# Optimization experiments

Measured on AMD Instinct MI355X. Metric: run time of the kernel, lower is better.

Reference implementation:

```python
import jax, jax.numpy as jnp
import numpy as np

def setup_inputs() -> dict:
    key = jax.random.key(0)
    k1, k2, k3, k4 = jax.random.split(key, 4)
    B, T, D = 4, 4096, 256
    # xavier_normal_ with gain 0.002: std = 0.002 * sqrt(2/(D+D))
    std = 0.002 * np.sqrt(2.0 / (D + D))
    return {
        "x": jax.random.normal(k1, (B, T, D), dtype=jnp.float32),
        "W_k": jax.random.normal(k2, (D, D), dtype=jnp.float32) * std,
        "W_q": jax.random.normal(k3, (D, D), dtype=jnp.float32) * std,
        "W_v": jax.random.normal(k4, (D, D), dtype=jnp.float32) * std,
    }

def reference(x, W_k, W_q, W_v):
    # Projections: (B,T,D) @ (D,D) -> (B,T,D)
    K = jnp.einsum('btd,dk->btk', x, W_k)
    Q = jnp.einsum('btd,dq->btq', x, W_q)
    V = jnp.einsum('btd,dv->btv', x, W_v)
    # Note: original code has NO 1/sqrt(D) scaling.
    scores = jnp.einsum('bqd,bkd->bqk', Q, K)  # (B,T,T)
    attn = jax.nn.softmax(scores, axis=2)
    return jnp.einsum('bta,bav->btv', attn, V)
```

## Files before the change

### kernel.cpp

```cpp
#include <hip/hip_runtime.h>

typedef __attribute__((ext_vector_type(4))) float f32x4;
typedef __attribute__((ext_vector_type(8))) __bf16 bf16x8;
typedef __attribute__((ext_vector_type(4))) unsigned short u16x4;
typedef unsigned short u16;
typedef unsigned int u32;
typedef unsigned long long u64;

#define AS1 __attribute__((address_space(1)))
#define AS3 __attribute__((address_space(3)))

__device__ __forceinline__ void gload_lds16(const void* g, void* l) {
  __builtin_amdgcn_global_load_lds((const AS1 u32*)g, (AS3 u32*)l, 16, 0, 0);
}

__global__ __launch_bounds__(256) void k_flag(float* __restrict__ out, int n) {
  for (int i = blockIdx.x * 256 + threadIdx.x; i < n; i += gridDim.x * 256)
    out[i] = 1.0f;
}

__global__ __launch_bounds__(256) void k_cvt_w(const float* __restrict__ Wk,
                                               const float* __restrict__ Wq,
                                               const float* __restrict__ Wv,
                                               __bf16* __restrict__ Wt) {
  const float* W = blockIdx.y == 0 ? Wk : (blockIdx.y == 1 ? Wq : Wv);
  int i = blockIdx.x * 256 + threadIdx.x;
  int n = i >> 8, k = i & 255;
  Wt[blockIdx.y * 65536 + i] = (__bf16)W[k * 256 + n];
}

__global__ __launch_bounds__(256) void k_proj(const float* __restrict__ x,
                                              const __bf16* __restrict__ Wt,
                                              __bf16* __restrict__ Kb,
                                              __bf16* __restrict__ Qb,
                                              __bf16* __restrict__ Vt) {
  __shared__ __bf16 As[128][72];
  __shared__ __bf16 Bs[128][72];
  int tid = threadIdx.x;
  int lane = tid & 63, w = tid >> 6;
  int l15 = lane & 15, l4 = lane >> 4;
  int m0 = blockIdx.x * 128, n0 = blockIdx.y * 128;
  int z = blockIdx.z;
  const __bf16* Wz = Wt + z * 65536;
  int wm = (w & 1) * 64, wn = (w >> 1) * 64;
  f32x4 acc[4][4];
  for (int a = 0; a < 4; ++a)
    for (int b = 0; b < 4; ++b) acc[a][b] = (f32x4){0.f, 0.f, 0.f, 0.f};

  for (int k0 = 0; k0 < 256; k0 += 64) {
    __syncthreads();
    for (int it = 0; it < 4; ++it) {
      int id = it * 256 + tid, r = id >> 3, c = id & 7;
      const float* src = x + (u64)(m0 + r) * 256 + k0 + c * 8;
      f32x4 a = *(const f32x4*)src, b2 = *(const f32x4*)(src + 4);
      bf16x8 o;
      o[0] = (__bf16)a[0];  o[1] = (__bf16)a[1];  o[2] = (__bf16)a[2];  o[3] = (__bf16)a[3];
      o[4] = (__bf16)b2[0]; o[5] = (__bf16)b2[1]; o[6] = (__bf16)b2[2]; o[7] = (__bf16)b2[3];
      *(bf16x8*)&As[r][c * 8] = o;
    }
    for (int it = 0; it < 4; ++it) {
      int id = it * 256 + tid, r = id >> 3, c = id & 7;
      *(bf16x8*)&Bs[r][c * 8] = *(const bf16x8*)(Wz + (u64)(n0 + r) * 256 + k0 + c * 8);
    }
    __syncthreads();
    for (int ks = 0; ks < 2; ++ks) {
      bf16x8 af[4], bg[4];
      for (int mf = 0; mf < 4; ++mf)
        af[mf] = *(const bf16x8*)&As[wm + mf * 16 + l15][(ks * 4 + l4) * 8];
      for (int nf = 0; nf < 4; ++nf)
        bg[nf] = *(const bf16x8*)&Bs[wn + nf * 16 + l15][(ks * 4 + l4) * 8];
      for (int mf = 0; mf < 4; ++mf)
        for (int nf = 0; nf < 4; ++nf)
          acc[mf][nf] = __builtin_amdgcn_mfma_f32_16x16x32_bf16(af[mf], bg[nf],
                                                                acc[mf][nf], 0, 0, 0);
    }
  }
  if (z != 2) {
    __bf16* C = z == 0 ? Kb : Qb;
    for (int mf = 0; mf < 4; ++mf)
      for (int nf = 0; nf < 4; ++nf)
        for (int r = 0; r < 4; ++r) {
          int m = m0 + wm + mf * 16 + l4 * 4 + r;
          int n = n0 + wn + nf * 16 + l15;
          C[(u64)m * 256 + n] = (__bf16)acc[mf][nf][r];
        }
  } else {
    int bb = m0 >> 12;
    for (int mf = 0; mf < 4; ++mf)
      for (int nf = 0; nf < 4; ++nf) {
        int n = n0 + wn + nf * 16 + l15;
        int tb = (m0 & 4095) + wm + mf * 16 + l4 * 4;
        u16x4 pk;
        for (int r = 0; r < 4; ++r) {
          __bf16 h = (__bf16)acc[mf][nf][r];
          pk[r] = __builtin_bit_cast(u16, h);
        }
        *(u16x4*)(Vt + (u64)bb * 1048576 + (u64)n * 4096 + tb) = pk;
      }
  }
}

#define KVB 32
__global__ __launch_bounds__(256) void k_attn(const __bf16* __restrict__ Qb,
                                              const __bf16* __restrict__ Kb,
                                              const __bf16* __restrict__ Vt,
                                              float* __restrict__ Out) {
  extern __shared__ char smem[];
  __bf16* Ks0 = (__bf16*)smem;
  __bf16* Ks1 = (__bf16*)(smem + 16384);
  __bf16* Vs0 = (__bf16*)(smem + 32768);
  __bf16* Vs1 = (__bf16*)(smem + 49152);
  __bf16* Ps  = (__bf16*)(smem + 65536);
  float*  Ls  = (float*)(smem + 69632);
  int tid = threadIdx.x, lane = tid & 63, w = tid >> 6;
  int l15 = lane & 15, l4 = lane >> 4;
  int id8 = blockIdx.x & 7, slot = blockIdx.x >> 3;
  int b = id8 >> 1;
  int q0 = (((id8 & 1) << 5) | slot) << 6;
  const __bf16* Kbb = Kb + (u64)b * 4096 * 256;
  const __bf16* Vtb = Vt + (u64)b * 1048576;

  const __bf16* Qrow = Qb + (u64)(b * 4096 + q0 + w * 16 + l15) * 256;
  bf16x8 qf[8];
  for (int ks = 0; ks < 8; ++ks) qf[ks] = *(const bf16x8*)(Qrow + ks * 32 + l4 * 8);

  f32x4 oacc[4][4];
  for (int a = 0; a < 4; ++a)
    for (int c = 0; c < 4; ++c) oacc[a][c] = (f32x4){0.f, 0.f, 0.f, 0.f};
  float lp[4] = {0.f, 0.f, 0.f, 0.f};

  auto stageK = [&](int kv0, __bf16* dst) {
    for (int it = 0; it < 4; ++it) {
      int id = it * 256 + tid;
      int r = id >> 5, c = id & 31, sc = c ^ (r & 7);
      gload_lds16(Kbb + (u64)(kv0 + r) * 256 + sc * 8, (char*)dst + id * 16);
    }
  };
  auto stageV = [&](int kv0, __bf16* dst) {
    for (int it = 0; it < 4; ++it) {
      int id = it * 256 + tid;
      int d = id >> 2, c = id & 3, sc = c ^ (d & 3);
      gload_lds16(Vtb + (u64)d * 4096 + kv0 + sc * 8, (char*)dst + id * 16);
    }
  };

  stageK(0, Ks0);
  stageV(0, Vs0);
  asm volatile("s_waitcnt vmcnt(0)" ::: "memory");
  __syncthreads();

  for (int t = 0; t < 128; ++t) {
    __bf16* Kc = (t & 1) ? Ks1 : Ks0;
    __bf16* Vc = (t & 1) ? Vs1 : Vs0;
    __bf16* Kn = (t & 1) ? Ks0 : Ks1;
    __bf16* Vn = (t & 1) ? Vs0 : Vs1;
    if (t < 127) { stageK((t + 1) * KVB, Kn); stageV((t + 1) * KVB, Vn); }

    f32x4 s0a = (f32x4){0.f, 0.f, 0.f, 0.f}, s0b = s0a, s1a = s0a, s1b = s0a;
    for (int ks = 0; ks < 8; ks += 2) {
      int ch00 = (ks * 4 + l4) ^ (l15 & 7);
      int ch10 = (ks * 4 + l4) ^ ((16 + l15) & 7);
      int ch01 = ((ks + 1) * 4 + l4) ^ (l15 & 7);
      int ch11 = ((ks + 1) * 4 + l4) ^ ((16 + l15) & 7);
      bf16x8 kf00 = *(const bf16x8*)((const char*)Kc + l15 * 512 + ch00 * 16);
      bf16x8 kf10 = *(const bf16x8*)((const char*)Kc + (16 + l15) * 512 + ch10 * 16);
      bf16x8 kf01 = *(const bf16x8*)((const char*)Kc + l15 * 512 + ch01 * 16);
      bf16x8 kf11 = *(const bf16x8*)((const char*)Kc + (16 + l15) * 512 + ch11 * 16);
      s0a = __builtin_amdgcn_mfma_f32_16x16x32_bf16(qf[ks], kf00, s0a, 0, 0, 0);
      s1a = __builtin_amdgcn_mfma_f32_16x16x32_bf16(qf[ks], kf10, s1a, 0, 0, 0);
      s0b = __builtin_amdgcn_mfma_f32_16x16x32_bf16(qf[ks + 1], kf01, s0b, 0, 0, 0);
      s1b = __builtin_amdgcn_mfma_f32_16x16x32_bf16(qf[ks + 1], kf11, s1b, 0, 0, 0);
    }
    f32x4 s0 = s0a + s0b, s1 = s1a + s1b;

    for (int r = 0; r < 4; ++r) {
      float p0 = __expf(s0[r]);
      float p1 = __expf(s1[r]);
      lp[r] += p0 + p1;
      int row = w * 16 + l4 * 4 + r;
      int c0 = (l15 >> 3) ^ (row & 3);
      Ps[row * 32 + c0 * 8 + (l15 & 7)] = (__bf16)p0;
      int c1 = ((16 + l15) >> 3) ^ (row & 3);
      Ps[row * 32 + c1 * 8 + (l15 & 7)] = (__bf16)p1;
    }
    asm volatile("s_waitcnt lgkmcnt(0)\n\ts_barrier" ::: "memory");

    bf16x8 vf[4];
    for (int nf = 0; nf < 4; ++nf) {
      int d = w * 64 + nf * 16 + l15;
      int vc = l4 ^ (d & 3);
      vf[nf] = *(const bf16x8*)((const char*)Vc + d * 64 + vc * 16);
    }
    for (int mf = 0; mf < 4; ++mf) {
      int qr = mf * 16 + l15;
      int pc = l4 ^ (qr & 3);
      bf16x8 pa = *(const bf16x8*)(Ps + qr * 32 + pc * 8);
      for (int nf = 0; nf < 4; ++nf)
        oacc[mf][nf] = __builtin_amdgcn_mfma_f32_16x16x32_bf16(pa, vf[nf], oacc[mf][nf], 0, 0, 0);
    }
    asm volatile("s_waitcnt vmcnt(0) lgkmcnt(0)\n\ts_barrier" ::: "memory");
  }

  for (int m = 1; m < 16; m <<= 1)
    for (int r = 0; r < 4; ++r) lp[r] += __shfl_xor(lp[r], m, 64);
  if (l15 == 0)
    for (int r = 0; r < 4; ++r) Ls[w * 16 + l4 * 4 + r] = lp[r];
  __syncthreads();

  float* Ob = Out + (u64)(b * 4096 + q0) * 256;
  for (int mf = 0; mf < 4; ++mf)
    for (int r = 0; r < 4; ++r) {
      float inv = 1.0f / Ls[mf * 16 + l4 * 4 + r];
      for (int nf = 0; nf < 4; ++nf)
        Ob[(u64)(mf * 16 + l4 * 4 + r) * 256 + w * 64 + nf * 16 + l15] =
            oacc[mf][nf][r] * inv;
    }
}

extern "C" void kernel_launch(void* const* d_in, const int* in_sizes, int n_in,
                              void* d_out, int out_size, void* d_ws, size_t ws_size,
                              hipStream_t stream) {
  const float* x  = (const float*)d_in[0];
  const float* Wk = (const float*)d_in[1];
  const float* Wq = (const float*)d_in[2];
  const float* Wv = (const float*)d_in[3];
  float* out = (float*)d_out;
  char* ws = (char*)d_ws;

  const size_t NEEDED = 25559040;
  if (ws_size < NEEDED) {
    k_flag<<<1024, 256, 0, stream>>>(out, out_size);
    return;
  }
  __bf16* Wt = (__bf16*)ws;
  __bf16* Kb = (__bf16*)(ws + 393216);
  __bf16* Qb = (__bf16*)(ws + 8781824);
  __bf16* Vt = (__bf16*)(ws + 17170432);

  k_cvt_w<<<dim3(256, 3), 256, 0, stream>>>(Wk, Wq, Wv, Wt);
  k_proj<<<dim3(128, 2, 3), 256, 0, stream>>>(x, Wt, Kb, Qb, Vt);
  k_attn<<<256, 256, 69888, stream>>>(Qb, Kb, Vt, out);
}
```

Before: 232.6 us.

## Halve attention query tile to 32 rows and pre-convert x to bf16 with async LDS loads

The attention kernel now gives each block 32 query rows instead of 64, doubling the grid to 512 blocks. The four waves split into two query halves times two key halves, and the two partial row sums are combined at the end. The projection kernel now reads a bf16 copy of x, produced by a new conversion kernel into the output buffer used as scratch, and stages tiles into swizzled LDS with global_load_lds. The aim is better CU occupancy and cheaper projection loads. The cost is that every block reloads K and V for fewer queries, doubling K/V traffic, plus one extra kernel launch.

```diff
diff --git a/kernel.cpp b/kernel.cpp
--- a/kernel.cpp
+++ b/kernel.cpp
@@ -17,6 +17,17 @@
 __global__ __launch_bounds__(256) void k_flag(float* __restrict__ out, int n) {
   for (int i = blockIdx.x * 256 + threadIdx.x; i < n; i += gridDim.x * 256)
     out[i] = 1.0f;
+}
+
+__global__ __launch_bounds__(256) void k_cvt_x(const float* __restrict__ x,
+                                               __bf16* __restrict__ xb) {
+  int i = blockIdx.x * 256 + threadIdx.x;
+  const f32x4* p = (const f32x4*)x;
+  f32x4 a = p[i * 2], b = p[i * 2 + 1];
+  bf16x8 o;
+  o[0] = (__bf16)a[0]; o[1] = (__bf16)a[1]; o[2] = (__bf16)a[2]; o[3] = (__bf16)a[3];
+  o[4] = (__bf16)b[0]; o[5] = (__bf16)b[1]; o[6] = (__bf16)b[2]; o[7] = (__bf16)b[3];
+  ((bf16x8*)xb)[i] = o;
 }
 
 __global__ __launch_bounds__(256) void k_cvt_w(const float* __restrict__ Wk,
@@ -29,13 +40,13 @@
   Wt[blockIdx.y * 65536 + i] = (__bf16)W[k * 256 + n];
 }
 
-__global__ __launch_bounds__(256) void k_proj(const float* __restrict__ x,
+__global__ __launch_bounds__(256) void k_proj(const __bf16* __restrict__ xb,
                                               const __bf16* __restrict__ Wt,
                                               __bf16* __restrict__ Kb,
                                               __bf16* __restrict__ Qb,
                                               __bf16* __restrict__ Vt) {
-  __shared__ __bf16 As[128][72];
-  __shared__ __bf16 Bs[128][72];
+  __shared__ __bf16 As[128 * 64];
+  __shared__ __bf16 Bs[128 * 64];
   int tid = threadIdx.x;
   int lane = tid & 63, w = tid >> 6;
   int l15 = lane & 15, l4 = lane >> 4;
@@ -50,25 +61,29 @@
   for (int k0 = 0; k0 < 256; k0 += 64) {
     __syncthreads();
     for (int it = 0; it < 4; ++it) {
-      int id = it * 256 + tid, r = id >> 3, c = id & 7;
-      const float* src = x + (u64)(m0 + r) * 256 + k0 + c * 8;
-      f32x4 a = *(const f32x4*)src, b2 = *(const f32x4*)(src + 4);
-      bf16x8 o;
-      o[0] = (__bf16)a[0];  o[1] = (__bf16)a[1];  o[2] = (__bf16)a[2];  o[3] = (__bf16)a[3];
-      o[4] = (__bf16)b2[0]; o[5] = (__bf16)b2[1]; o[6] = (__bf16)b2[2]; o[7] = (__bf16)b2[3];
-      *(bf16x8*)&As[r][c * 8] = o;
-    }
-    for (int it = 0; it < 4; ++it) {
-      int id = it * 256 + tid, r = id >> 3, c = id & 7;
-      *(bf16x8*)&Bs[r][c * 8] = *(const bf16x8*)(Wz + (u64)(n0 + r) * 256 + k0 + c * 8);
-    }
+      int id = it * 256 + tid;
+      int r = id >> 3, c = id & 7, sc = c ^ (r & 7);
+      gload_lds16(xb + (u64)(m0 + r) * 256 + k0 + sc * 8, (char*)As + id * 16);
+    }
+    for (int it = 0; it < 4; ++it) {
+      int id = it * 256 + tid;
+      int r = id >> 3, c = id & 7, sc = c ^ (r & 7);
+      gload_lds16(Wz + (u64)(n0 + r) * 256 + k0 + sc * 8, (char*)Bs + id * 16);
+    }
+    asm volatile("s_waitcnt vmcnt(0)" ::: "memory");
     __syncthreads();
     for (int ks = 0; ks < 2; ++ks) {
       bf16x8 af[4], bg[4];
-      for (int mf = 0; mf < 4; ++mf)
-        af[mf] = *(const bf16x8*)&As[wm + mf * 16 + l15][(ks * 4 + l4) * 8];
-      for (int nf = 0; nf < 4; ++nf)
-        bg[nf] = *(const bf16x8*)&Bs[wn + nf * 16 + l15][(ks * 4 + l4) * 8];
+      for (int mf = 0; mf < 4; ++mf) {
+        int m = wm + mf * 16 + l15;
+        int ch = (ks * 4 + l4) ^ (m & 7);
+        af[mf] = *(const bf16x8*)((const char*)As + m * 128 + ch * 16);
+      }
+      for (int nf = 0; nf < 4; ++nf) {
+        int n = wn + nf * 16 + l15;
+        int ch = (ks * 4 + l4) ^ (n & 7);
+        bg[nf] = *(const bf16x8*)((const char*)Bs + n * 128 + ch * 16);
+      }
       for (int mf = 0; mf < 4; ++mf)
         for (int nf = 0; nf < 4; ++nf)
           acc[mf][nf] = __builtin_amdgcn_mfma_f32_16x16x32_bf16(af[mf], bg[nf],
@@ -111,21 +126,22 @@
   __bf16* Vs0 = (__bf16*)(smem + 32768);
   __bf16* Vs1 = (__bf16*)(smem + 49152);
   __bf16* Ps  = (__bf16*)(smem + 65536);
-  float*  Ls  = (float*)(smem + 69632);
+  float*  Ls  = (float*)(smem + 67584);
   int tid = threadIdx.x, lane = tid & 63, w = tid >> 6;
   int l15 = lane & 15, l4 = lane >> 4;
+  int s = w & 1, h = w >> 1;
   int id8 = blockIdx.x & 7, slot = blockIdx.x >> 3;
   int b = id8 >> 1;
-  int q0 = (((id8 & 1) << 5) | slot) << 6;
+  int q0 = (((id8 & 1) << 6) | slot) << 5;
   const __bf16* Kbb = Kb + (u64)b * 4096 * 256;
   const __bf16* Vtb = Vt + (u64)b * 1048576;
 
-  const __bf16* Qrow = Qb + (u64)(b * 4096 + q0 + w * 16 + l15) * 256;
+  const __bf16* Qrow = Qb + (u64)(b * 4096 + q0 + s * 16 + l15) * 256;
   bf16x8 qf[8];
   for (int ks = 0; ks < 8; ++ks) qf[ks] = *(const bf16x8*)(Qrow + ks * 32 + l4 * 8);
 
-  f32x4 oacc[4][4];
-  for (int a = 0; a < 4; ++a)
+  f32x4 oacc[2][4];
+  for (int a = 0; a < 2; ++a)
     for (int c = 0; c < 4; ++c) oacc[a][c] = (f32x4){0.f, 0.f, 0.f, 0.f};
   float lp[4] = {0.f, 0.f, 0.f, 0.f};
 
@@ -156,32 +172,25 @@
     __bf16* Vn = (t & 1) ? Vs0 : Vs1;
     if (t < 127) { stageK((t + 1) * KVB, Kn); stageV((t + 1) * KVB, Vn); }
 
-    f32x4 s0a = (f32x4){0.f, 0.f, 0.f, 0.f}, s0b = s0a, s1a = s0a, s1b = s0a;
+    int kr = h * 16 + l15;
+    f32x4 sa = (f32x4){0.f, 0.f, 0.f, 0.f}, sb = sa;
     for (int ks = 0; ks < 8; ks += 2) {
-      int ch00 = (ks * 4 + l4) ^ (l15 & 7);
-      int ch10 = (ks * 4 + l4) ^ ((16 + l15) & 7);
-      int ch01 = ((ks + 1) * 4 + l4) ^ (l15 & 7);
-      int ch11 = ((ks + 1) * 4 + l4) ^ ((16 + l15) & 7);
-      bf16x8 kf00 = *(const bf16x8*)((const char*)Kc + l15 * 512 + ch00 * 16);
-      bf16x8 kf10 = *(const bf16x8*)((const char*)Kc + (16 + l15) * 512 + ch10 * 16);
-      bf16x8 kf01 = *(const bf16x8*)((const char*)Kc + l15 * 512 + ch01 * 16);
-      bf16x8 kf11 = *(const bf16x8*)((const char*)Kc + (16 + l15) * 512 + ch11 * 16);
-      s0a = __builtin_amdgcn_mfma_f32_16x16x32_bf16(qf[ks], kf00, s0a, 0, 0, 0);
-      s1a = __builtin_amdgcn_mfma_f32_16x16x32_bf16(qf[ks], kf10, s1a, 0, 0, 0);
-      s0b = __builtin_amdgcn_mfma_f32_16x16x32_bf16(qf[ks + 1], kf01, s0b, 0, 0, 0);
-      s1b = __builtin_amdgcn_mfma_f32_16x16x32_bf16(qf[ks + 1], kf11, s1b, 0, 0, 0);
-    }
-    f32x4 s0 = s0a + s0b, s1 = s1a + s1b;
+      int ch0 = (ks * 4 + l4) ^ (kr & 7);
+      int ch1 = ((ks + 1) * 4 + l4) ^ (kr & 7);
+      bf16x8 kf0 = *(const bf16x8*)((const char*)Kc + kr * 512 + ch0 * 16);
+      bf16x8 kf1 = *(const bf16x8*)((const char*)Kc + kr * 512 + ch1 * 16);
+      sa = __builtin_amdgcn_mfma_f32_16x16x32_bf16(qf[ks], kf0, sa, 0, 0, 0);
+      sb = __builtin_amdgcn_mfma_f32_16x16x32_bf16(qf[ks + 1], kf1, sb, 0, 0, 0);
+    }
+    f32x4 sv = sa + sb;
 
     for (int r = 0; r < 4; ++r) {
-      float p0 = __expf(s0[r]);
-      float p1 = __expf(s1[r]);
-      lp[r] += p0 + p1;
-      int row = w * 16 + l4 * 4 + r;
-      int c0 = (l15 >> 3) ^ (row & 3);
-      Ps[row * 32 + c0 * 8 + (l15 & 7)] = (__bf16)p0;
-      int c1 = ((16 + l15) >> 3) ^ (row & 3);
-      Ps[row * 32 + c1 * 8 + (l15 & 7)] = (__bf16)p1;
+      float p = __expf(sv[r]);
+      lp[r] += p;
+      int row = s * 16 + l4 * 4 + r;
+      int ch = h * 2 + (l15 >> 3);
+      int sc = ch ^ (row & 3);
+      Ps[row * 32 + sc * 8 + (l15 & 7)] = (__bf16)p;
     }
     asm volatile("s_waitcnt lgkmcnt(0)\n\ts_barrier" ::: "memory");
 
@@ -191,7 +200,7 @@
       int vc = l4 ^ (d & 3);
       vf[nf] = *(const bf16x8*)((const char*)Vc + d * 64 + vc * 16);
     }
-    for (int mf = 0; mf < 4; ++mf) {
+    for (int mf = 0; mf < 2; ++mf) {
       int qr = mf * 16 + l15;
       int pc = l4 ^ (qr & 3);
       bf16x8 pa = *(const bf16x8*)(Ps + qr * 32 + pc * 8);
@@ -204,16 +213,16 @@
   for (int m = 1; m < 16; m <<= 1)
     for (int r = 0; r < 4; ++r) lp[r] += __shfl_xor(lp[r], m, 64);
   if (l15 == 0)
-    for (int r = 0; r < 4; ++r) Ls[w * 16 + l4 * 4 + r] = lp[r];
+    for (int r = 0; r < 4; ++r) Ls[h * 32 + s * 16 + l4 * 4 + r] = lp[r];
   __syncthreads();
 
   float* Ob = Out + (u64)(b * 4096 + q0) * 256;
-  for (int mf = 0; mf < 4; ++mf)
+  for (int mf = 0; mf < 2; ++mf)
     for (int r = 0; r < 4; ++r) {
-      float inv = 1.0f / Ls[mf * 16 + l4 * 4 + r];
+      int row = mf * 16 + l4 * 4 + r;
+      float inv = 1.0f / (Ls[row] + Ls[32 + row]);
       for (int nf = 0; nf < 4; ++nf)
-        Ob[(u64)(mf * 16 + l4 * 4 + r) * 256 + w * 64 + nf * 16 + l15] =
-            oacc[mf][nf][r] * inv;
+        Ob[(u64)row * 256 + w * 64 + nf * 16 + l15] = oacc[mf][nf][r] * inv;
     }
 }
 
@@ -236,8 +245,10 @@
   __bf16* Kb = (__bf16*)(ws + 393216);
   __bf16* Qb = (__bf16*)(ws + 8781824);
   __bf16* Vt = (__bf16*)(ws + 17170432);
-
+  __bf16* xb = (__bf16*)d_out;
+
+  k_cvt_x<<<2048, 256, 0, stream>>>(x, xb);
   k_cvt_w<<<dim3(256, 3), 256, 0, stream>>>(Wk, Wq, Wv, Wt);
-  k_proj<<<dim3(128, 2, 3), 256, 0, stream>>>(x, Wt, Kb, Qb, Vt);
-  k_attn<<<256, 256, 69888, stream>>>(Qb, Kb, Vt, out);
-}
+  k_proj<<<dim3(128, 2, 3), 256, 0, stream>>>(xb, Wt, Kb, Qb, Vt);
+  k_attn<<<512, 256, 67840, stream>>>(Qb, Kb, Vt, out);
+}
```

Result: no change. 233.9 us (+0.6%).
